# Kernel tuning notes

Hardware: AMD Instinct MI355X
Metric: run time of the kernel (lower is better)

The kernel has to match this reference:

```python
import jax, jax.numpy as jnp
import numpy as np

WINDOW_SIZE = 11
CHANNEL = 3
SIGMA = 1.5
C1 = 0.01 ** 2
C2 = 0.03 ** 2


def _gaussian_window():
    # 1D gaussian, normalized, then outer product -> [C,1,K,K] depthwise kernel
    x = np.arange(WINDOW_SIZE, dtype=np.float32)
    g = np.exp(-(x - WINDOW_SIZE // 2) ** 2 / (2.0 * SIGMA ** 2))
    g = g / g.sum()
    w2d = np.outer(g, g).astype(np.float32)  # [K,K]
    w = np.broadcast_to(w2d, (CHANNEL, 1, WINDOW_SIZE, WINDOW_SIZE)).copy()
    return jnp.asarray(w)


def _depthwise_conv(x, w):
    # x: [N,C,H,W], w: [C,1,K,K]; SAME padding (pad = K//2, K odd) matches torch
    pad = WINDOW_SIZE // 2
    return jax.lax.conv_general_dilated(
        x, w,
        window_strides=(1, 1),
        padding=((pad, pad), (pad, pad)),
        dimension_numbers=("NCHW", "OIHW", "NCHW"),
        feature_group_count=CHANNEL,
    )


def setup_inputs() -> dict:
    key = jax.random.key(0)
    kA, kB = jax.random.split(key)
    shape = (16, 3, 512, 512)
    A = jax.random.uniform(kA, shape, dtype=jnp.float32)
    B = jax.random.uniform(kB, shape, dtype=jnp.float32)
    return {"A": A, "B": B}


def reference(A, B):
    w = _gaussian_window()
    mu1 = _depthwise_conv(A, w)
    mu2 = _depthwise_conv(B, w)
    mu1_sq = mu1 * mu1
    mu2_sq = mu2 * mu2
    mu12 = mu1 * mu2
    sigma1_sq = _depthwise_conv(A * A, w) - mu1_sq
    sigma2_sq = _depthwise_conv(B * B, w) - mu2_sq
    sigma12 = _depthwise_conv(A * B, w) - mu12
    num = (2.0 * mu12 + C1) * (2.0 * sigma12 + C2)
    den = (mu1_sq + mu2_sq + C1) * (sigma1_sq + sigma2_sq + C2)
    ssim_map = num / den
    return jnp.nanmean(ssim_map)
```

## Files before the change

### kernel.cpp

```cpp
#include <hip/hip_runtime.h>
#include <math.h>


#define IMG 512
#define C1F 1.0e-4f
#define C2F 9.0e-4f

#define SR 42
#define RS 259

#define NBLK 6144

__global__ void ssim_finalize(const double* __restrict__ part, float* __restrict__ out) {
    const int t = threadIdx.x;
    double v = 0.0;
    #pragma unroll
    for (int i = 0; i < NBLK / 256; ++i)
        v += part[t + 256 * i];
    #pragma unroll
    for (int off = 32; off > 0; off >>= 1)
        v += __shfl_down(v, off, 64);
    __shared__ double w[4];
    if ((t & 63) == 0) w[t >> 6] = v;
    __syncthreads();
    if (t == 0)
        *out = (float)((w[0] + w[1] + w[2] + w[3]) / 12582912.0);
}

__device__ __forceinline__ void make_weights(float* g) {
    float e[6];
    #pragma unroll
    for (int k = 0; k < 6; ++k) {
        const float d = (float)k;
        e[k] = expf(-d * d / 4.5f);
    }
    float gs = e[5];
    gs += e[4]; gs += e[3]; gs += e[2]; gs += e[1]; gs += e[0];
    gs += e[1]; gs += e[2]; gs += e[3]; gs += e[4]; gs += e[5];
    float q[6];
    #pragma unroll
    for (int k = 0; k < 6; ++k) q[k] = e[k] / gs;
    #pragma unroll
    for (int i = 0; i < 11; ++i) {
        const int d = (i < 5) ? (5 - i) : (i - 5);
        g[i] = q[d];
    }
}

__global__ __launch_bounds__(256, 3)
void ssim_main(const float* __restrict__ A, const float* __restrict__ B,
               double* __restrict__ part)
{
    __shared__ float hbuf[SR * RS];

    const int t  = threadIdx.x;
    const int x0 = blockIdx.x * 64;
    const int y0 = blockIdx.y * 32;
    const size_t pbase = (size_t)blockIdx.z * (size_t)(IMG * IMG);
    const float* __restrict__ pa = A + pbase;
    const float* __restrict__ pb = B + pbase;

    float g[11];
    make_weights(g);

    if (t < 252) {
        const int r = t / 6;
        const int s = t - 6 * r;
        const int start = (s == 5) ? 53 : s * 11;
        const int gy  = y0 - 5 + r;
        const int gx0 = x0 + start - 5;
        const bool rowok = ((unsigned)gy < (unsigned)IMG);
        const float* __restrict__ ra = pa + (ptrdiff_t)gy * IMG;
        const float* __restrict__ rb = pb + (ptrdiff_t)gy * IMG;

        float wa[21], wb[21];
        if (rowok && gx0 >= 0 && gx0 + 20 < IMG) {
            #pragma unroll
            for (int j = 0; j < 21; ++j) {
                wa[j] = ra[gx0 + j];
                wb[j] = rb[gx0 + j];
            }
        } else {
            #pragma unroll
            for (int j = 0; j < 21; ++j) {
                const int gx = gx0 + j;
                const bool ok = rowok && ((unsigned)gx < (unsigned)IMG);
                wa[j] = ok ? ra[gx] : 0.f;
                wb[j] = ok ? rb[gx] : 0.f;
            }
        }

        float sa[11], sb[11], ss[11], sp[11];
        #pragma unroll
        for (int p = 0; p < 11; ++p)
        { sa[p]=0.f; sb[p]=0.f; ss[p]=0.f; sp[p]=0.f; }
        #pragma unroll
        for (int m = 0; m < 21; ++m) {
            const float a = wa[m];
            const float b = wb[m];
            const float s2v = a * a + b * b;
            const float ab  = a * b;
            #pragma unroll
            for (int p = 0; p < 11; ++p) {
                const int k = m - p;
                if (k >= 0 && k <= 10) {
                    const float w = g[k];
                    sa[p] += w * a;   sb[p] += w * b;
                    ss[p] += w * s2v; sp[p] += w * ab;
                }
            }
        }

        const int base = r * RS + start;
        #pragma unroll
        for (int p = 0; p < 11; ++p) {
            hbuf[base + p]        = sa[p];
            hbuf[base + 65 + p]   = sb[p];
            hbuf[base + 130 + p]  = ss[p];
            hbuf[base + 195 + p]  = sp[p];
        }
    }
    __syncthreads();

    float lsum = 0.f;
    {
        const int x  = t & 63;
        const int yb = (t >> 6) << 3;
        float m1[8], m2[8], es[8], ep[8];
        #pragma unroll
        for (int j = 0; j < 8; ++j)
        { m1[j]=0.f; m2[j]=0.f; es[j]=0.f; ep[j]=0.f; }

        #pragma unroll
        for (int k = 0; k < 18; ++k) {
            const int o = (yb + k) * RS + x;
            const float vA = hbuf[o];
            const float vB = hbuf[o + 65];
            const float vS = hbuf[o + 130];
            const float vP = hbuf[o + 195];
            #pragma unroll
            for (int j = 0; j < 8; ++j) {
                const int kk = k - j;
                if (kk >= 0 && kk <= 10) {
                    const float w = g[kk];
                    m1[j] += w * vA; m2[j] += w * vB;
                    es[j] += w * vS; ep[j] += w * vP;
                }
            }
        }

        #pragma unroll
        for (int j = 0; j < 8; ++j) {
            const float mu1 = m1[j], mu2 = m2[j];
            const float mu1s = mu1 * mu1, mu2s = mu2 * mu2, mu12 = mu1 * mu2;
            const float s12  = ep[j] - mu12;
            const float ssum = es[j] - mu1s - mu2s;
            const float num = (2.f * mu12 + C1F) * (2.f * s12 + C2F);
            const float den = (mu1s + mu2s + C1F) * (ssum + C2F);
            float rd = __builtin_amdgcn_rcpf(den);
            rd = rd * (2.f - den * rd);
            lsum += num * rd;
        }
    }

    #pragma unroll
    for (int off = 32; off > 0; off >>= 1)
        lsum += __shfl_down(lsum, off, 64);

    __syncthreads();
    if ((t & 63) == 0) hbuf[t >> 6] = lsum;
    __syncthreads();
    if (t == 0) {
        const double bs = (double)hbuf[0] + (double)hbuf[1]
                        + (double)hbuf[2] + (double)hbuf[3];
        const int slot = blockIdx.x + (blockIdx.y << 3) + (blockIdx.z << 7);
        part[slot] = bs;
    }
}

extern "C" void kernel_launch(void* const* d_in, const int* in_sizes, int n_in,
                              void* d_out, int out_size, void* d_ws, size_t ws_size,
                              hipStream_t stream) {
    const float* A = (const float*)d_in[0];
    const float* B = (const float*)d_in[1];
    float* out   = (float*)d_out;
    double* part = (double*)d_ws;

    dim3 grid(IMG / 64, IMG / 32, 48);
    ssim_main<<<grid, dim3(256), 0, stream>>>(A, B, part);
    ssim_finalize<<<dim3(1), dim3(256), 0, stream>>>(part, out);
}
```

Before: 158.8 us.

## Interleave horizontal sums as float4 in LDS and pass weights as kernel args

Stores the four horizontal-pass results (A, B, squares, product) interleaved as one float4 per pixel in shared memory, so each thread writes and reads a single 128-bit LDS access instead of four scalar ones. The row stride changes to 260 to keep float4 alignment. The Gaussian weights are now computed once on the host in double precision and passed by value as kernel arguments, so the per-thread expf and division work goes away. The 16-byte-per-lane pattern may cause different LDS bank conflicts, and the weights now live in scalar registers loaded from the kernel argument segment.

```diff
diff --git a/kernel.cpp b/kernel.cpp
--- a/kernel.cpp
+++ b/kernel.cpp
@@ -6,10 +6,12 @@
 #define C1F 1.0e-4f
 #define C2F 9.0e-4f
 
-#define SR 42
-#define RS 259
+#define SR  42
+#define RSF 260
 
 #define NBLK 6144
+
+struct GW { float g[11]; };
 
 __global__ void ssim_finalize(const double* __restrict__ part, float* __restrict__ out) {
     const int t = threadIdx.x;
@@ -27,31 +29,11 @@
         *out = (float)((w[0] + w[1] + w[2] + w[3]) / 12582912.0);
 }
 
-__device__ __forceinline__ void make_weights(float* g) {
-    float e[6];
-    #pragma unroll
-    for (int k = 0; k < 6; ++k) {
-        const float d = (float)k;
-        e[k] = expf(-d * d / 4.5f);
-    }
-    float gs = e[5];
-    gs += e[4]; gs += e[3]; gs += e[2]; gs += e[1]; gs += e[0];
-    gs += e[1]; gs += e[2]; gs += e[3]; gs += e[4]; gs += e[5];
-    float q[6];
-    #pragma unroll
-    for (int k = 0; k < 6; ++k) q[k] = e[k] / gs;
-    #pragma unroll
-    for (int i = 0; i < 11; ++i) {
-        const int d = (i < 5) ? (5 - i) : (i - 5);
-        g[i] = q[d];
-    }
-}
-
 __global__ __launch_bounds__(256, 3)
 void ssim_main(const float* __restrict__ A, const float* __restrict__ B,
-               double* __restrict__ part)
+               double* __restrict__ part, const GW gw)
 {
-    __shared__ float hbuf[SR * RS];
+    __shared__ float hbuf[SR * RSF];
 
     const int t  = threadIdx.x;
     const int x0 = blockIdx.x * 64;
@@ -59,9 +41,6 @@
     const size_t pbase = (size_t)blockIdx.z * (size_t)(IMG * IMG);
     const float* __restrict__ pa = A + pbase;
     const float* __restrict__ pb = B + pbase;
-
-    float g[11];
-    make_weights(g);
 
     if (t < 252) {
         const int r = t / 6;
@@ -104,20 +83,18 @@
             for (int p = 0; p < 11; ++p) {
                 const int k = m - p;
                 if (k >= 0 && k <= 10) {
-                    const float w = g[k];
+                    const float w = gw.g[k];
                     sa[p] += w * a;   sb[p] += w * b;
                     ss[p] += w * s2v; sp[p] += w * ab;
                 }
             }
         }
 
-        const int base = r * RS + start;
+        const int base = r * RSF;
         #pragma unroll
         for (int p = 0; p < 11; ++p) {
-            hbuf[base + p]        = sa[p];
-            hbuf[base + 65 + p]   = sb[p];
-            hbuf[base + 130 + p]  = ss[p];
-            hbuf[base + 195 + p]  = sp[p];
+            *(float4*)&hbuf[base + (start + p) * 4] =
+                make_float4(sa[p], sb[p], ss[p], sp[p]);
         }
     }
     __syncthreads();
@@ -133,18 +110,14 @@
 
         #pragma unroll
         for (int k = 0; k < 18; ++k) {
-            const int o = (yb + k) * RS + x;
-            const float vA = hbuf[o];
-            const float vB = hbuf[o + 65];
-            const float vS = hbuf[o + 130];
-            const float vP = hbuf[o + 195];
+            const float4 q = *(const float4*)&hbuf[(yb + k) * RSF + x * 4];
             #pragma unroll
             for (int j = 0; j < 8; ++j) {
                 const int kk = k - j;
                 if (kk >= 0 && kk <= 10) {
-                    const float w = g[kk];
-                    m1[j] += w * vA; m2[j] += w * vB;
-                    es[j] += w * vS; ep[j] += w * vP;
+                    const float w = gw.g[kk];
+                    m1[j] += w * q.x; m2[j] += w * q.y;
+                    es[j] += w * q.z; ep[j] += w * q.w;
                 }
             }
         }
@@ -186,7 +159,18 @@
     float* out   = (float*)d_out;
     double* part = (double*)d_ws;
 
+    GW gw;
+    {
+        double e[11], s = 0.0;
+        for (int i = 0; i < 11; ++i) {
+            const double d = (double)(i - 5);
+            e[i] = exp(-d * d / 4.5);
+            s += e[i];
+        }
+        for (int i = 0; i < 11; ++i) gw.g[i] = (float)(e[i] / s);
+    }
+
     dim3 grid(IMG / 64, IMG / 32, 48);
-    ssim_main<<<grid, dim3(256), 0, stream>>>(A, B, part);
+    ssim_main<<<grid, dim3(256), 0, stream>>>(A, B, part, gw);
     ssim_finalize<<<dim3(1), dim3(256), 0, stream>>>(part, out);
 }
```

Measured after the change: 159.0 us. Within noise of the previous version (+0.1%).
